# Kernel optimization log

Measured on AMD Instinct MI355X. Metric: run time of the kernel, lower is better.

The kernel has to match this reference:

```python
import jax, jax.numpy as jnp
import numpy as np

V, E, S_MAX, H, L = 32000, 1024, 2048, 16, 6
D = E // H  # head_dim = 64
EPS = 1e-5


def _ln(x, g, b):
    mu = jnp.mean(x, axis=-1, keepdims=True)
    var = jnp.mean(jnp.square(x - mu), axis=-1, keepdims=True)
    return (x - mu) * jax.lax.rsqrt(var + EPS) * g + b


def setup_inputs() -> dict:
    key = jax.random.key(0)
    ks = iter(jax.random.split(key, 32))
    std = 0.02
    B, S = 1, 2048
    inp = {
        "tokens": jax.random.randint(next(ks), (B, S), 0, V, dtype=jnp.int32),
        "W_emb": jax.random.normal(next(ks), (V, E), jnp.float32) * std,  # tied with fc_out
        "W_pos": jax.random.normal(next(ks), (S_MAX, E), jnp.float32) * std,
        # per-layer stacked params [L, ...]
        "Wq": jax.random.normal(next(ks), (L, E, E), jnp.float32) * std,
        "Wk": jax.random.normal(next(ks), (L, E, E), jnp.float32) * std,
        "Wv": jax.random.normal(next(ks), (L, E, E), jnp.float32) * std,
        "Wo": jax.random.normal(next(ks), (L, E, E), jnp.float32) * std,
        "bo": jnp.zeros((L, E), jnp.float32),
        "ln1_g": jnp.ones((L, E), jnp.float32),
        "ln1_b": jnp.zeros((L, E), jnp.float32),
        "ln2_g": jnp.ones((L, E), jnp.float32),
        "ln2_b": jnp.zeros((L, E), jnp.float32),
        "W1": jax.random.normal(next(ks), (L, 4 * E, E), jnp.float32) * std,
        "b1": jnp.zeros((L, 4 * E), jnp.float32),
        "W2": jax.random.normal(next(ks), (L, E, 4 * E), jnp.float32) * std,
        "b2": jnp.zeros((L, E), jnp.float32),
        "lnf_g": jnp.ones((E,), jnp.float32),
        "lnf_b": jnp.zeros((E,), jnp.float32),
    }
    return inp


def _gpt_forward(tokens, W_emb, W_pos, Wq, Wk, Wv, Wo, bo, ln1_g, ln1_b,
                 ln2_g, ln2_b, W1, b1, W2, b2, lnf_g, lnf_b):
    B, S = tokens.shape
    x = W_emb[tokens] + W_pos[:S][None, :, :]  # [B,S,E]
    causal = jnp.tril(jnp.ones((S, S), bool))  # [S,S]
    scale = 1.0 / np.sqrt(D)

    def block(x, p):
        wq, wk, wv, wo, bo_, g1, b1n, g2, b2n, w1, bf1, w2, bf2 = p
        h = _ln(x, g1, b1n)
        # torch Linear: y = x @ W.T ; split heads -> [B,H,S,D]
        def heads(w):
            return (h @ w.T).reshape(B, S, H, D).transpose(0, 2, 1, 3)
        q, k, v = heads(wq), heads(wk), heads(wv)
        scores = jnp.einsum('bhqd,bhkd->bhqk', q, k) * scale
        scores = jnp.where(causal[None, None], scores, -jnp.inf)
        attn = jax.nn.softmax(scores, axis=-1)
        o = jnp.einsum('bhqk,bhkd->bhqd', attn, v)
        o = o.transpose(0, 2, 1, 3).reshape(B, S, E)
        x = x + o @ wo.T + bo_
        h2 = _ln(x, g2, b2n)
        ff = jax.nn.gelu(h2 @ w1.T + bf1, approximate=False) @ w2.T + bf2
        return x + ff, None

    params = (Wq, Wk, Wv, Wo, bo, ln1_g, ln1_b, ln2_g, ln2_b, W1, b1, W2, b2)
    x, _ = jax.lax.scan(block, x, params)
    x = _ln(x, lnf_g, lnf_b)
    return x @ W_emb.T  # tied output projection [B,S,V]


def reference(tokens, W_emb, W_pos, Wq, Wk, Wv, Wo, bo, ln1_g, ln1_b,
              ln2_g, ln2_b, W1, b1, W2, b2, lnf_g, lnf_b):
    return _gpt_forward(tokens, W_emb, W_pos, Wq, Wk, Wv, Wo, bo, ln1_g,
                        ln1_b, ln2_g, ln2_b, W1, b1, W2, b2, lnf_g, lnf_b)
```

## Files before the change

### kernel.cpp

```cpp
#include <hip/hip_runtime.h>
#include <math.h>

#define S_LEN 2048
#define EMB 1024
#define NHEAD 16
#define HDIM 64
#define NLAYER 6
#define VOCAB 32000
#define FFDIM 4096

using f32x4 = __attribute__((ext_vector_type(4))) float;
using bf16x8 = __attribute__((ext_vector_type(8))) __bf16;
typedef unsigned short us;

static __device__ __forceinline__ unsigned short f2bf(float f) {
  union { float f; unsigned int u; } v; v.f = f;
  unsigned int r = v.u + 0x7FFFu + ((v.u >> 16) & 1u);
  return (unsigned short)(r >> 16);
}

#define GLOAD_LDS16(g, l)                                                      \
  __builtin_amdgcn_global_load_lds(                                            \
      (const __attribute__((address_space(1))) void*)(g),                      \
      (__attribute__((address_space(3))) void*)(l), 16, 0, 0)

__global__ __launch_bounds__(256) void cvt_bf16_kernel(
    const float* __restrict__ in, us* __restrict__ out, long n) {
  long i = ((long)blockIdx.x * 256 + threadIdx.x) * 8;
  if (i >= n) return;
  const float4* p = (const float4*)(in + i);
  float4 a = p[0], b = p[1];
  uint4 o;
  o.x = (unsigned)f2bf(a.x) | ((unsigned)f2bf(a.y) << 16);
  o.y = (unsigned)f2bf(a.z) | ((unsigned)f2bf(a.w) << 16);
  o.z = (unsigned)f2bf(b.x) | ((unsigned)f2bf(b.y) << 16);
  o.w = (unsigned)f2bf(b.z) | ((unsigned)f2bf(b.w) << 16);
  *(uint4*)(out + i) = o;
}

__global__ __launch_bounds__(256) void embed_kernel(
    const int* __restrict__ tok, const float* __restrict__ Wemb,
    const float* __restrict__ Wpos, float* __restrict__ x) {
  int s = blockIdx.x, t = threadIdx.x;
  int tk = tok[s];
  const float4* we = (const float4*)(Wemb + (size_t)tk * EMB);
  const float4* wp = (const float4*)(Wpos + (size_t)s * EMB);
  float4 a = we[t], b = wp[t];
  float4 o; o.x = a.x + b.x; o.y = a.y + b.y; o.z = a.z + b.z; o.w = a.w + b.w;
  ((float4*)(x + (size_t)s * EMB))[t] = o;
}

__global__ __launch_bounds__(256) void ln_kernel(
    const float* __restrict__ x, const float* __restrict__ g,
    const float* __restrict__ b, us* __restrict__ out) {
  int row = blockIdx.x, t = threadIdx.x, lane = t & 63, wave = t >> 6;
  float4 v = ((const float4*)(x + (size_t)row * EMB))[t];
  float s = v.x + v.y + v.z + v.w;
  float q = v.x * v.x + v.y * v.y + v.z * v.z + v.w * v.w;
  #pragma unroll
  for (int d = 1; d < 64; d <<= 1) { s += __shfl_xor(s, d); q += __shfl_xor(q, d); }
  __shared__ float rs[4], rq[4];
  if (lane == 0) { rs[wave] = s; rq[wave] = q; }
  __syncthreads();
  s = rs[0] + rs[1] + rs[2] + rs[3];
  q = rq[0] + rq[1] + rq[2] + rq[3];
  float mean = s * (1.0f / EMB);
  float var = q * (1.0f / EMB) - mean * mean;
  float rstd = rsqrtf(var + 1e-5f);
  float4 gg = ((const float4*)g)[t], bb = ((const float4*)b)[t];
  ushort4 o;
  o.x = f2bf((v.x - mean) * rstd * gg.x + bb.x);
  o.y = f2bf((v.y - mean) * rstd * gg.y + bb.y);
  o.z = f2bf((v.z - mean) * rstd * gg.z + bb.z);
  o.w = f2bf((v.w - mean) * rstd * gg.w + bb.w);
  ((ushort4*)(out + (size_t)row * EMB))[t] = o;
}

template <int SK>
__global__ __launch_bounds__(256) void reduce_ln_kernel(
    float* __restrict__ x, const float* __restrict__ p,
    const float* __restrict__ bias, const float* __restrict__ g,
    const float* __restrict__ b, us* __restrict__ out) {
  int row = blockIdx.x, t = threadIdx.x, lane = t & 63, wave = t >> 6;
  const size_t plane = (size_t)S_LEN * EMB;
  float4 v = ((const float4*)(x + (size_t)row * EMB))[t];
  float4 bb4 = ((const float4*)bias)[t];
  v.x += bb4.x; v.y += bb4.y; v.z += bb4.z; v.w += bb4.w;
  #pragma unroll
  for (int z = 0; z < SK; ++z) {
    float4 q4 = ((const float4*)(p + z * plane + (size_t)row * EMB))[t];
    v.x += q4.x; v.y += q4.y; v.z += q4.z; v.w += q4.w;
  }
  ((float4*)(x + (size_t)row * EMB))[t] = v;
  float s = v.x + v.y + v.z + v.w;
  float q = v.x * v.x + v.y * v.y + v.z * v.z + v.w * v.w;
  #pragma unroll
  for (int d = 1; d < 64; d <<= 1) { s += __shfl_xor(s, d); q += __shfl_xor(q, d); }
  __shared__ float rs[4], rq[4];
  if (lane == 0) { rs[wave] = s; rq[wave] = q; }
  __syncthreads();
  s = rs[0] + rs[1] + rs[2] + rs[3];
  q = rq[0] + rq[1] + rq[2] + rq[3];
  float mean = s * (1.0f / EMB);
  float var = q * (1.0f / EMB) - mean * mean;
  float rstd = rsqrtf(var + 1e-5f);
  float4 gg = ((const float4*)g)[t], lb = ((const float4*)b)[t];
  ushort4 o;
  o.x = f2bf((v.x - mean) * rstd * gg.x + lb.x);
  o.y = f2bf((v.y - mean) * rstd * gg.y + lb.y);
  o.z = f2bf((v.z - mean) * rstd * gg.z + lb.z);
  o.w = f2bf((v.w - mean) * rstd * gg.w + lb.w);
  ((ushort4*)(out + (size_t)row * EMB))[t] = o;
}

#define STAGE_R(MATP, BROW, LDSB, TT)                                          \
  {                                                                            \
    const int kk0 = (TT) << 5;                                                 \
    _Pragma("unroll")                                                          \
    for (int i_ = 0; i_ < 2; ++i_) {                                           \
      const int ci = t + i_ * 256;                                             \
      const int rr = ci >> 2, cc = ci & 3;                                     \
      const int src = (cc ^ ((rr >> 1) & 3)) * 8;                              \
      GLOAD_LDS16(MATP + (size_t)((BROW) + rr) * K + kk0 + src,                \
                  &LDSB[0] + (wave * 64 + i_ * 256) * 8);                      \
    }                                                                          \
  }

template <int HAS_BIAS, int DO_GELU, int OUT_BF16>
__global__ __launch_bounds__(256) void gemm_r128(
    const us* __restrict__ A, const us* __restrict__ B0,
    const us* __restrict__ B1, const us* __restrict__ B2,
    const float* __restrict__ bias,
    void* C0, void* C1, void* C2, int M, int N, int K) {
  const us* B = blockIdx.z == 0 ? B0 : (blockIdx.z == 1 ? B1 : B2);
  void* C = blockIdx.z == 0 ? C0 : (blockIdx.z == 1 ? C1 : C2);
  const int nwg = gridDim.x * gridDim.y;
  int lin = blockIdx.y * gridDim.x + blockIdx.x;
  {
    const int qx = nwg >> 3, r = nwg & 7;
    const int xcd = lin & 7, idx = lin >> 3;
    lin = (xcd < r ? xcd * (qx + 1) : r * (qx + 1) + (xcd - r) * qx) + idx;
  }
  const int m0 = (lin % gridDim.x) * 128, n0 = (lin / gridDim.x) * 128;
  const int t = threadIdx.x, lane = t & 63, wave = t >> 6;
  const int lq = lane & 15, hi = lane >> 4;
  const int wm = (wave >> 1) * 64, wn = (wave & 1) * 64;
  __shared__ __align__(16) us As[3][128 * 32];
  __shared__ __align__(16) us Bs[3][128 * 32];
  f32x4 acc[4][4] = {};
  const int nt = K >> 5;

  STAGE_R(A, m0, As[0], 0); STAGE_R(B, n0, Bs[0], 0);
  STAGE_R(A, m0, As[1], 1); STAGE_R(B, n0, Bs[1], 1);
  STAGE_R(A, m0, As[2], 2); STAGE_R(B, n0, Bs[2], 2);
  asm volatile("s_waitcnt vmcnt(8)" ::: "memory");
  __builtin_amdgcn_s_barrier();
  __builtin_amdgcn_sched_barrier(0);

  int bb = 0;
  for (int tt = 0; tt < nt; ++tt) {
    const int sb = (bb + 2 >= 3) ? bb - 1 : bb + 2;
    const us* Ab = &As[bb][0];
    const us* Bb = &Bs[bb][0];
    bf16x8 a[4], b[4];
    #pragma unroll
    for (int f = 0; f < 4; ++f) {
      const int row = wm + f * 16 + lq;
      a[f] = *(const bf16x8*)(Ab + row * 32 + ((hi ^ ((row >> 1) & 3)) * 8));
    }
    #pragma unroll
    for (int f = 0; f < 4; ++f) {
      const int row = wn + f * 16 + lq;
      b[f] = *(const bf16x8*)(Bb + row * 32 + ((hi ^ ((row >> 1) & 3)) * 8));
    }
    if (tt + 2 < nt) {
      STAGE_R(A, m0, As[sb], tt + 2);
      STAGE_R(B, n0, Bs[sb], tt + 2);
    }
    __builtin_amdgcn_s_setprio(1);
    #pragma unroll
    for (int i = 0; i < 4; ++i)
      #pragma unroll
      for (int j = 0; j < 4; ++j)
        acc[i][j] = __builtin_amdgcn_mfma_f32_16x16x32_bf16(a[i], b[j], acc[i][j], 0, 0, 0);
    __builtin_amdgcn_s_setprio(0);
    if (tt + 2 < nt) {
      asm volatile("s_waitcnt vmcnt(4)" ::: "memory");
    } else {
      asm volatile("s_waitcnt vmcnt(0)" ::: "memory");
    }
    __builtin_amdgcn_s_barrier();
    __builtin_amdgcn_sched_barrier(0);
    bb = (bb + 1 == 3) ? 0 : bb + 1;
  }
  const int r0 = hi * 4;
  #pragma unroll
  for (int i = 0; i < 4; ++i) {
    #pragma unroll
    for (int j = 0; j < 4; ++j) {
      const int col = n0 + wn + j * 16 + lq;
      float bv = HAS_BIAS ? bias[col] : 0.0f;
      #pragma unroll
      for (int r = 0; r < 4; ++r) {
        const int row = m0 + wm + i * 16 + r0 + r;
        float val = acc[i][j][r] + bv;
        if (DO_GELU) val = val * 0.5f * (1.0f + erff(val * 0.70710678118f));
        if (OUT_BF16) ((us*)C)[(size_t)row * N + col] = f2bf(val);
        else          ((float*)C)[(size_t)row * N + col] = val;
      }
    }
  }
}

__global__ __launch_bounds__(256) void gemm_rsk(
    const us* __restrict__ A, const us* __restrict__ B,
    float* __restrict__ C, int M, int N, int K, int kSlice) {
  const int z = blockIdx.z;
  const int nwg = gridDim.x * gridDim.y;
  int lin = blockIdx.y * gridDim.x + blockIdx.x;
  {
    const int qx = nwg >> 3, r = nwg & 7;
    const int xcd = lin & 7, idx = lin >> 3;
    lin = (xcd < r ? xcd * (qx + 1) : r * (qx + 1) + (xcd - r) * qx) + idx;
  }
  const int m0 = (lin % gridDim.x) * 128, n0 = (lin / gridDim.x) * 128;
  const int t = threadIdx.x, lane = t & 63, wave = t >> 6;
  const int lq = lane & 15, hi = lane >> 4;
  const int wm = (wave >> 1) * 64, wn = (wave & 1) * 64;
  __shared__ __align__(16) us As[3][128 * 32];
  __shared__ __align__(16) us Bs[3][128 * 32];
  f32x4 acc[4][4] = {};
  const int nt = kSlice >> 5;
  const int tb = z * (kSlice >> 5);

  STAGE_R(A, m0, As[0], tb + 0); STAGE_R(B, n0, Bs[0], tb + 0);
  STAGE_R(A, m0, As[1], tb + 1); STAGE_R(B, n0, Bs[1], tb + 1);
  STAGE_R(A, m0, As[2], tb + 2); STAGE_R(B, n0, Bs[2], tb + 2);
  asm volatile("s_waitcnt vmcnt(8)" ::: "memory");
  __builtin_amdgcn_s_barrier();
  __builtin_amdgcn_sched_barrier(0);

  int bb = 0;
  for (int tt = 0; tt < nt; ++tt) {
    const int sb = (bb + 2 >= 3) ? bb - 1 : bb + 2;
    const us* Ab = &As[bb][0];
    const us* Bb = &Bs[bb][0];
    bf16x8 a[4], b[4];
    #pragma unroll
    for (int f = 0; f < 4; ++f) {
      const int row = wm + f * 16 + lq;
      a[f] = *(const bf16x8*)(Ab + row * 32 + ((hi ^ ((row >> 1) & 3)) * 8));
    }
    #pragma unroll
    for (int f = 0; f < 4; ++f) {
      const int row = wn + f * 16 + lq;
      b[f] = *(const bf16x8*)(Bb + row * 32 + ((hi ^ ((row >> 1) & 3)) * 8));
    }
    if (tt + 2 < nt) {
      STAGE_R(A, m0, As[sb], tb + tt + 2);
      STAGE_R(B, n0, Bs[sb], tb + tt + 2);
    }
    __builtin_amdgcn_s_setprio(1);
    #pragma unroll
    for (int i = 0; i < 4; ++i)
      #pragma unroll
      for (int j = 0; j < 4; ++j)
        acc[i][j] = __builtin_amdgcn_mfma_f32_16x16x32_bf16(a[i], b[j], acc[i][j], 0, 0, 0);
    __builtin_amdgcn_s_setprio(0);
    if (tt + 2 < nt) {
      asm volatile("s_waitcnt vmcnt(4)" ::: "memory");
    } else {
      asm volatile("s_waitcnt vmcnt(0)" ::: "memory");
    }
    __builtin_amdgcn_s_barrier();
    __builtin_amdgcn_sched_barrier(0);
    bb = (bb + 1 == 3) ? 0 : bb + 1;
  }
  float* Cz = C + (size_t)z * M * N;
  #pragma unroll
  for (int i = 0; i < 4; ++i)
    #pragma unroll
    for (int j = 0; j < 4; ++j) {
      const int col = n0 + wn + j * 16 + lq;
      #pragma unroll
      for (int r = 0; r < 4; ++r)
        Cz[(size_t)(m0 + wm + i * 16 + hi * 4 + r) * N + col] = acc[i][j][r];
    }
}

__global__ __launch_bounds__(512, 1) void gemm_v8p(
    const us* __restrict__ A, const us* __restrict__ B,
    float* __restrict__ C, int M, int N, int K) {
  const int nwg = gridDim.x * gridDim.y;
  int lin = blockIdx.y * gridDim.x + blockIdx.x;
  {
    const int qx = nwg >> 3, r = nwg & 7;
    const int xcd = lin & 7, idx = lin >> 3;
    lin = (xcd < r ? xcd * (qx + 1) : r * (qx + 1) + (xcd - r) * qx) + idx;
  }
  const int m0 = (lin % gridDim.x) * 256, n0 = (lin / gridDim.x) * 256;
  const int t = threadIdx.x, lane = t & 63, wave = t >> 6;
  const int lq = lane & 15, hi = lane >> 4;
  const int rbase = (wave >> 2) * 128, cbase = (wave & 3) * 64;
  __shared__ __align__(16) us As[3][256 * 32];
  __shared__ __align__(16) us Bs[3][256 * 32];
  f32x4 acc[8][4] = {};
  const int nt = K >> 5;

#define STAGE_T(MAT, LDSB, TT)                                                 \
  {                                                                            \
    const int kk0 = (TT) << 5;                                                 \
    _Pragma("unroll")                                                          \
    for (int i_ = 0; i_ < 2; ++i_) {                                           \
      const int ci = t + i_ * 512;                                             \
      const int rr = ci >> 2, cc = ci & 3;                                     \
      const int src = (cc ^ ((rr >> 1) & 3)) * 8;                              \
      GLOAD_LDS16(MAT + (size_t)(((MAT == A) ? m0 : n0) + rr) * K + kk0 + src, \
                  &LDSB[0] + (wave * 64 + i_ * 512) * 8);                      \
    }                                                                          \
  }

  STAGE_T(A, As[0], 0); STAGE_T(B, Bs[0], 0);
  STAGE_T(A, As[1], 1); STAGE_T(B, Bs[1], 1);
  STAGE_T(A, As[2], 2); STAGE_T(B, Bs[2], 2);
  asm volatile("s_waitcnt vmcnt(8)" ::: "memory");
  __builtin_amdgcn_s_barrier();
  __builtin_amdgcn_sched_barrier(0);

  int bb = 0;
  for (int tt = 0; tt < nt; ++tt) {
    const int sb = (bb + 2 >= 3) ? bb - 1 : bb + 2;
    const us* Ab = &As[bb][0];
    const us* Bb = &Bs[bb][0];
    bf16x8 a0[4], a1[4], b0[4];
    #pragma unroll
    for (int f = 0; f < 4; ++f) {
      const int row = rbase + f * 16 + lq;
      a0[f] = *(const bf16x8*)(Ab + row * 32 + ((hi ^ ((row >> 1) & 3)) * 8));
    }
    #pragma unroll
    for (int f = 0; f < 4; ++f) {
      const int row = rbase + 64 + f * 16 + lq;
      a1[f] = *(const bf16x8*)(Ab + row * 32 + ((hi ^ ((row >> 1) & 3)) * 8));
    }
    #pragma unroll
    for (int f = 0; f < 4; ++f) {
      const int row = cbase + f * 16 + lq;
      b0[f] = *(const bf16x8*)(Bb + row * 32 + ((hi ^ ((row >> 1) & 3)) * 8));
    }
    if (tt + 2 < nt) {
      STAGE_T(A, As[sb], tt + 2);
      STAGE_T(B, Bs[sb], tt + 2);
    }
    __builtin_amdgcn_s_setprio(1);
    #pragma unroll
    for (int i = 0; i < 4; ++i)
      #pragma unroll
      for (int j = 0; j < 4; ++j)
        acc[i][j] = __builtin_amdgcn_mfma_f32_16x16x32_bf16(a0[i], b0[j], acc[i][j], 0, 0, 0);
    #pragma unroll
    for (int i = 0; i < 4; ++i)
      #pragma unroll
      for (int j = 0; j < 4; ++j)
        acc[4 + i][j] = __builtin_amdgcn_mfma_f32_16x16x32_bf16(a1[i], b0[j], acc[4 + i][j], 0, 0, 0);
    __builtin_amdgcn_s_setprio(0);
    if (tt + 2 < nt) {
      asm volatile("s_waitcnt vmcnt(4)" ::: "memory");
    } else {
      asm volatile("s_waitcnt vmcnt(0)" ::: "memory");
    }
    __builtin_amdgcn_s_barrier();
    __builtin_amdgcn_sched_barrier(0);
    bb = (bb + 1 == 3) ? 0 : bb + 1;
  }
#undef STAGE_T
  #pragma unroll
  for (int i = 0; i < 8; ++i)
    #pragma unroll
    for (int j = 0; j < 4; ++j) {
      const int col = n0 + cbase + j * 16 + lq;
      #pragma unroll
      for (int r = 0; r < 4; ++r)
        C[(size_t)(m0 + rbase + i * 16 + hi * 4 + r) * N + col] = acc[i][j][r];
    }
}

__global__ __launch_bounds__(256) void attn_kernel(
    const us* __restrict__ qb, const us* __restrict__ kb,
    const us* __restrict__ vb, us* __restrict__ ob) {
  const int qt = gridDim.x - 1 - blockIdx.x;
  const int head = blockIdx.y;
  const int t = threadIdx.x, lane = t & 63, wave = t >> 6;
  const int hi = lane >> 4, lq = lane & 15;
  const int hd = head * HDIM;
  const int q0w = qt * 64 + wave * 16;
  __shared__ __align__(16) us Kl[2][64 * 64];
  __shared__ __align__(16) us Vl[2][64 * 72];
  __shared__ __align__(16) us Pl[4][16][72];
  bf16x8 qf[2];
  {
    const us* qp = qb + (size_t)(q0w + lq) * EMB + hd + hi * 8;
    qf[0] = *(const bf16x8*)qp;
    qf[1] = *(const bf16x8*)(qp + 32);
    #pragma unroll
    for (int e = 0; e < 8; ++e) {
      qf[0][e] = (__bf16)((float)qf[0][e] * 0.125f);
      qf[1][e] = (__bf16)((float)qf[1][e] * 0.125f);
    }
  }
  f32x4 accO[4] = {};
  float m_run = -1e30f, l_run = 0.f;
  const int vr2 = (t >> 3) * 2, d8 = (t & 7) * 8;
  const int q_g = q0w + lq;

  {
    #pragma unroll
    for (int i = 0; i < 2; ++i) {
      const int c = wave * 64 + lane + i * 256;
      const int row = c >> 3, j = c & 7;
      const int colE = (j * 8) ^ ((row & 7) << 3);
      GLOAD_LDS16(kb + (size_t)(row) * EMB + hd + colE,
                  &Kl[0][0] + (wave * 64 + i * 256) * 8);
    }
    const us* vp = vb + (size_t)vr2 * EMB + hd + d8;
    uint4 vA = *(const uint4*)vp;
    uint4 vB = *(const uint4*)(vp + EMB);
    const unsigned* wa = (const unsigned*)&vA;
    const unsigned* wb = (const unsigned*)&vB;
    #pragma unroll
    for (int i = 0; i < 8; ++i) {
      unsigned lo = (i & 1) ? (wa[i >> 1] >> 16) : (wa[i >> 1] & 0xffffu);
      unsigned hw = (i & 1) ? (wb[i >> 1] >> 16) : (wb[i >> 1] & 0xffffu);
      *(unsigned*)(&Vl[0][0] + (d8 + i) * 72 + vr2) = lo | (hw << 16);
    }
  }
  __syncthreads();
  int cur = 0;
  for (int kt = 0; kt <= qt; ++kt) {
    uint4 vA, vB;
    if (kt < qt) {
      #pragma unroll
      for (int i = 0; i < 2; ++i) {
        const int c = wave * 64 + lane + i * 256;
        const int row = c >> 3, j = c & 7;
        const int colE = (j * 8) ^ ((row & 7) << 3);
        GLOAD_LDS16(kb + (size_t)((kt + 1) * 64 + row) * EMB + hd + colE,
                    &Kl[cur ^ 1][0] + (wave * 64 + i * 256) * 8);
      }
      const us* vp = vb + (size_t)((kt + 1) * 64 + vr2) * EMB + hd + d8;
      vA = *(const uint4*)vp;
      vB = *(const uint4*)(vp + EMB);
    }
    f32x4 sc[4] = {};
    #pragma unroll
    for (int ks = 0; ks < 2; ++ks) {
      #pragma unroll
      for (int fn = 0; fn < 4; ++fn) {
        const int rowk = fn * 16 + lq;
        const us* kp = &Kl[cur][0] + rowk * 64 + ((ks * 32 + hi * 8) ^ ((rowk & 7) << 3));
        sc[fn] = __builtin_amdgcn_mfma_f32_16x16x32_bf16(
            *(const bf16x8*)kp, qf[ks], sc[fn], 0, 0, 0);
      }
    }
    float pv[16];
    float pmax = -1e30f;
    if (kt == qt) {
      #pragma unroll
      for (int fn = 0; fn < 4; ++fn)
        #pragma unroll
        for (int r = 0; r < 4; ++r) {
          const int k_g = kt * 64 + fn * 16 + hi * 4 + r;
          float sv = sc[fn][r];
          if (k_g > q_g) sv = -1e30f;
          pv[fn * 4 + r] = sv;
          pmax = fmaxf(pmax, sv);
        }
    } else {
      #pragma unroll
      for (int fn = 0; fn < 4; ++fn)
        #pragma unroll
        for (int r = 0; r < 4; ++r) {
          float sv = sc[fn][r];
          pv[fn * 4 + r] = sv;
          pmax = fmaxf(pmax, sv);
        }
    }
    pmax = fmaxf(pmax, __shfl_xor(pmax, 16));
    pmax = fmaxf(pmax, __shfl_xor(pmax, 32));
    if (!__all(pmax <= m_run + 8.0f)) {
      const float mn = fmaxf(m_run, pmax);
      const float alpha = __expf(m_run - mn);
      m_run = mn;
      l_run *= alpha;
      float ar[4];
      #pragma unroll
      for (int r = 0; r < 4; ++r) ar[r] = __shfl(alpha, hi * 4 + r);
      #pragma unroll
      for (int df = 0; df < 4; ++df)
        #pragma unroll
        for (int r = 0; r < 4; ++r) accO[df][r] *= ar[r];
    }
    float rsum = 0.f;
    #pragma unroll
    for (int i = 0; i < 16; ++i) {
      float e = __expf(pv[i] - m_run);
      pv[i] = e;
      rsum += e;
    }
    rsum += __shfl_xor(rsum, 16);
    rsum += __shfl_xor(rsum, 32);
    l_run += rsum;
    #pragma unroll
    for (int fn = 0; fn < 4; ++fn) {
      ushort4 pk;
      pk.x = f2bf(pv[fn * 4 + 0]);
      pk.y = f2bf(pv[fn * 4 + 1]);
      pk.z = f2bf(pv[fn * 4 + 2]);
      pk.w = f2bf(pv[fn * 4 + 3]);
      *(ushort4*)&Pl[wave][lq][fn * 16 + hi * 4] = pk;
    }
    #pragma unroll
    for (int ks = 0; ks < 2; ++ks) {
      bf16x8 pf = *(const bf16x8*)&Pl[wave][lq][ks * 32 + hi * 8];
      #pragma unroll
      for (int df = 0; df < 4; ++df) {
        bf16x8 vf = *(const bf16x8*)(&Vl[cur][0] + (df * 16 + lq) * 72 + ks * 32 + hi * 8);
        accO[df] = __builtin_amdgcn_mfma_f32_16x16x32_bf16(pf, vf, accO[df], 0, 0, 0);
      }
    }
    if (kt < qt) {
      const unsigned* wa = (const unsigned*)&vA;
      const unsigned* wb = (const unsigned*)&vB;
      #pragma unroll
      for (int i = 0; i < 8; ++i) {
        unsigned lo = (i & 1) ? (wa[i >> 1] >> 16) : (wa[i >> 1] & 0xffffu);
        unsigned hw = (i & 1) ? (wb[i >> 1] >> 16) : (wb[i >> 1] & 0xffffu);
        *(unsigned*)(&Vl[cur ^ 1][0] + (d8 + i) * 72 + vr2) = lo | (hw << 16);
      }
    }
    __syncthreads();
    cur ^= 1;
  }
  float linv[4];
  #pragma unroll
  for (int r = 0; r < 4; ++r) linv[r] = 1.0f / __shfl(l_run, hi * 4 + r);
  #pragma unroll
  for (int r = 0; r < 4; ++r) {
    const int row = q0w + hi * 4 + r;
    #pragma unroll
    for (int df = 0; df < 4; ++df)
      ob[(size_t)row * EMB + hd + df * 16 + lq] = f2bf(accO[df][r] * linv[r]);
  }
}

extern "C" void kernel_launch(void* const* d_in, const int* in_sizes, int n_in,
                              void* d_out, int out_size, void* d_ws, size_t ws_size,
                              hipStream_t stream) {
  const int* tok = (const int*)d_in[0];
  const float* Wemb = (const float*)d_in[1];
  const float* Wpos = (const float*)d_in[2];
  const float* Wq = (const float*)d_in[3];
  const float* Wk = (const float*)d_in[4];
  const float* Wv = (const float*)d_in[5];
  const float* Wo = (const float*)d_in[6];
  const float* bo = (const float*)d_in[7];
  const float* ln1g = (const float*)d_in[8];
  const float* ln1b = (const float*)d_in[9];
  const float* ln2g = (const float*)d_in[10];
  const float* ln2b = (const float*)d_in[11];
  const float* W1 = (const float*)d_in[12];
  const float* b1 = (const float*)d_in[13];
  const float* W2 = (const float*)d_in[14];
  const float* b2 = (const float*)d_in[15];
  const float* lnfg = (const float*)d_in[16];
  const float* lnfb = (const float*)d_in[17];
  (void)in_sizes; (void)n_in; (void)out_size;

  const size_t MB = 1u << 20;
  char* ws = (char*)d_ws;
  float* x = (float*)ws;
  us* h  = (us*)(ws + 8 * MB);
  us* qb = (us*)(ws + 12 * MB);
  us* kb = (us*)(ws + 16 * MB);
  us* vb = (us*)(ws + 20 * MB);
  us* ob = (us*)(ws + 24 * MB);
  us* fb = (us*)(ws + 12 * MB);
  us* cWq = (us*)(ws + 28 * MB);
  us* cWk = (us*)(ws + 40 * MB);
  us* cWv = (us*)(ws + 52 * MB);
  us* cWo = (us*)(ws + 64 * MB);
  us* cW1 = (us*)(ws + 76 * MB);
  us* cW2 = (us*)(ws + 124 * MB);
  us* cWemb = (us*)(ws + 172 * MB);
  float* pbuf = (float*)(ws + 236 * MB);
  const size_t need = 236 * MB + 32 * MB;
  if (ws_size < need) {
    embed_kernel<<<dim3(S_LEN), 256, 0, stream>>>(tok, Wemb, Wpos, x);
    return;
  }

  embed_kernel<<<dim3(S_LEN), 256, 0, stream>>>(tok, Wemb, Wpos, x);

  const long nE2 = (long)NLAYER * EMB * EMB;
  const long nF  = (long)NLAYER * FFDIM * EMB;
  const long nV  = (long)VOCAB * EMB;
  cvt_bf16_kernel<<<(int)(nE2 / 2048), 256, 0, stream>>>(Wq, cWq, nE2);
  cvt_bf16_kernel<<<(int)(nE2 / 2048), 256, 0, stream>>>(Wk, cWk, nE2);
  cvt_bf16_kernel<<<(int)(nE2 / 2048), 256, 0, stream>>>(Wv, cWv, nE2);
  cvt_bf16_kernel<<<(int)(nE2 / 2048), 256, 0, stream>>>(Wo, cWo, nE2);
  cvt_bf16_kernel<<<(int)(nF / 2048), 256, 0, stream>>>(W1, cW1, nF);
  cvt_bf16_kernel<<<(int)(nF / 2048), 256, 0, stream>>>(W2, cW2, nF);
  cvt_bf16_kernel<<<(int)(nV / 2048), 256, 0, stream>>>(Wemb, cWemb, nV);

  ln_kernel<<<S_LEN, 256, 0, stream>>>(x, ln1g, ln1b, h);
  for (int l = 0; l < NLAYER; ++l) {
    const size_t wofs = (size_t)l * EMB * EMB;
    const size_t fofs = (size_t)l * FFDIM * EMB;
    gemm_r128<0, 0, 1><<<dim3(16, 8, 3), 256, 0, stream>>>(
        h, cWq + wofs, cWk + wofs, cWv + wofs, nullptr,
        qb, kb, vb, S_LEN, EMB, EMB);
    attn_kernel<<<dim3(32, NHEAD), 256, 0, stream>>>(qb, kb, vb, ob);
    gemm_rsk<<<dim3(16, 8, 2), 256, 0, stream>>>(
        ob, cWo + wofs, pbuf, S_LEN, EMB, EMB, EMB / 2);
    reduce_ln_kernel<2><<<S_LEN, 256, 0, stream>>>(
        x, pbuf, bo + l * EMB, ln2g + l * EMB, ln2b + l * EMB, h);
    gemm_r128<1, 1, 1><<<dim3(16, 32, 1), 256, 0, stream>>>(
        h, cW1 + fofs, nullptr, nullptr, b1 + l * FFDIM,
        fb, nullptr, nullptr, S_LEN, FFDIM, EMB);
    gemm_rsk<<<dim3(16, 8, 4), 256, 0, stream>>>(
        fb, cW2 + fofs, pbuf, S_LEN, EMB, FFDIM, FFDIM / 4);
    if (l < NLAYER - 1)
      reduce_ln_kernel<4><<<S_LEN, 256, 0, stream>>>(
          x, pbuf, b2 + l * EMB, ln1g + (l + 1) * EMB, ln1b + (l + 1) * EMB, h);
    else
      reduce_ln_kernel<4><<<S_LEN, 256, 0, stream>>>(
          x, pbuf, b2 + l * EMB, lnfg, lnfb, h);
  }
  gemm_v8p<<<dim3(8, 125), 512, 0, stream>>>(
      h, cWemb, (float*)d_out, S_LEN, VOCAB, EMB);
}
```

Measured before the change: 1.382 ms.

## Load K fragments directly from global in attention and use exp2 softmax

Drops the double-buffered LDS staging of K tiles in the attention kernel. Each wave now loads its K MFMA fragments straight from global memory every iteration, with no prefetch of the next tile. It also folds log2(e) into the query scale so softmax can use exp2f in place of __expf. This removes LDS traffic and shared memory pressure, but every wave now re-reads K from global memory and global load latency is exposed inside the loop.

```diff
diff --git a/kernel.cpp b/kernel.cpp
--- a/kernel.cpp
+++ b/kernel.cpp
@@ -394,7 +394,6 @@
   const int hi = lane >> 4, lq = lane & 15;
   const int hd = head * HDIM;
   const int q0w = qt * 64 + wave * 16;
-  __shared__ __align__(16) us Kl[2][64 * 64];
   __shared__ __align__(16) us Vl[2][64 * 72];
   __shared__ __align__(16) us Pl[4][16][72];
   bf16x8 qf[2];
@@ -404,8 +403,8 @@
     qf[1] = *(const bf16x8*)(qp + 32);
     #pragma unroll
     for (int e = 0; e < 8; ++e) {
-      qf[0][e] = (__bf16)((float)qf[0][e] * 0.125f);
-      qf[1][e] = (__bf16)((float)qf[1][e] * 0.125f);
+      qf[0][e] = (__bf16)((float)qf[0][e] * 0.18033688f);
+      qf[1][e] = (__bf16)((float)qf[1][e] * 0.18033688f);
     }
   }
   f32x4 accO[4] = {};
@@ -414,14 +413,6 @@
   const int q_g = q0w + lq;
 
   {
-    #pragma unroll
-    for (int i = 0; i < 2; ++i) {
-      const int c = wave * 64 + lane + i * 256;
-      const int row = c >> 3, j = c & 7;
-      const int colE = (j * 8) ^ ((row & 7) << 3);
-      GLOAD_LDS16(kb + (size_t)(row) * EMB + hd + colE,
-                  &Kl[0][0] + (wave * 64 + i * 256) * 8);
-    }
     const us* vp = vb + (size_t)vr2 * EMB + hd + d8;
     uint4 vA = *(const uint4*)vp;
     uint4 vB = *(const uint4*)(vp + EMB);
@@ -439,29 +430,24 @@
   for (int kt = 0; kt <= qt; ++kt) {
     uint4 vA, vB;
     if (kt < qt) {
-      #pragma unroll
-      for (int i = 0; i < 2; ++i) {
-        const int c = wave * 64 + lane + i * 256;
-        const int row = c >> 3, j = c & 7;
-        const int colE = (j * 8) ^ ((row & 7) << 3);
-        GLOAD_LDS16(kb + (size_t)((kt + 1) * 64 + row) * EMB + hd + colE,
-                    &Kl[cur ^ 1][0] + (wave * 64 + i * 256) * 8);
-      }
       const us* vp = vb + (size_t)((kt + 1) * 64 + vr2) * EMB + hd + d8;
       vA = *(const uint4*)vp;
       vB = *(const uint4*)(vp + EMB);
     }
+    const us* kpb = kb + (size_t)(kt * 64 + lq) * EMB + hd + hi * 8;
+    bf16x8 kf0[4], kf1[4];
+    #pragma unroll
+    for (int fn = 0; fn < 4; ++fn) {
+      kf0[fn] = *(const bf16x8*)(kpb + (size_t)fn * 16 * EMB);
+      kf1[fn] = *(const bf16x8*)(kpb + (size_t)fn * 16 * EMB + 32);
+    }
     f32x4 sc[4] = {};
     #pragma unroll
-    for (int ks = 0; ks < 2; ++ks) {
-      #pragma unroll
-      for (int fn = 0; fn < 4; ++fn) {
-        const int rowk = fn * 16 + lq;
-        const us* kp = &Kl[cur][0] + rowk * 64 + ((ks * 32 + hi * 8) ^ ((rowk & 7) << 3));
-        sc[fn] = __builtin_amdgcn_mfma_f32_16x16x32_bf16(
-            *(const bf16x8*)kp, qf[ks], sc[fn], 0, 0, 0);
-      }
-    }
+    for (int fn = 0; fn < 4; ++fn)
+      sc[fn] = __builtin_amdgcn_mfma_f32_16x16x32_bf16(kf0[fn], qf[0], sc[fn], 0, 0, 0);
+    #pragma unroll
+    for (int fn = 0; fn < 4; ++fn)
+      sc[fn] = __builtin_amdgcn_mfma_f32_16x16x32_bf16(kf1[fn], qf[1], sc[fn], 0, 0, 0);
     float pv[16];
     float pmax = -1e30f;
     if (kt == qt) {
@@ -489,7 +475,7 @@
     pmax = fmaxf(pmax, __shfl_xor(pmax, 32));
     if (!__all(pmax <= m_run + 8.0f)) {
       const float mn = fmaxf(m_run, pmax);
-      const float alpha = __expf(m_run - mn);
+      const float alpha = exp2f(m_run - mn);
       m_run = mn;
       l_run *= alpha;
       float ar[4];
@@ -503,7 +489,7 @@
     float rsum = 0.f;
     #pragma unroll
     for (int i = 0; i < 16; ++i) {
-      float e = __expf(pv[i] - m_run);
+      float e = exp2f(pv[i] - m_run);
       pv[i] = e;
       rsum += e;
     }
```

Result: slower. 1.526 ms (+10.4%).
